# Kernel optimization log

Measured on AMD Instinct MI355X. Metric: run time of the kernel, lower is better.

Reference implementation:

```python
import jax, jax.numpy as jnp
import numpy as np

DIM = 64
N_ITER = 2
NUM_USR = 50000
NUM_ENT = 200000
NUM_REL = 32
N_NEIGHBOR = 16
BATCH = 4096


def setup_inputs() -> dict:
    key = jax.random.key(0)
    ks = jax.random.split(key, 12)
    u = jax.random.randint(ks[0], (BATCH,), 0, NUM_USR)
    v = jax.random.randint(ks[1], (BATCH,), 0, NUM_ENT)
    adj = jax.random.randint(ks[2], (NUM_ENT, N_NEIGHBOR), 0, NUM_ENT)
    rel_adj = jax.random.randint(ks[3], (NUM_ENT, N_NEIGHBOR), 0, NUM_REL + 1)
    usr_emb = jax.random.normal(ks[4], (NUM_USR, DIM), dtype=jnp.float32)
    ent_emb = jax.random.normal(ks[5], (NUM_ENT, DIM), dtype=jnp.float32)
    rel_emb = jax.random.normal(ks[6], (NUM_REL + 1, DIM), dtype=jnp.float32)
    # per-hop aggregator Linear(dim, dim) weights (applied as x @ W + b)
    scale = 1.0 / np.sqrt(DIM)
    W0 = jax.random.uniform(ks[7], (DIM, DIM), jnp.float32, -scale, scale)
    b0 = jax.random.uniform(ks[8], (DIM,), jnp.float32, -scale, scale)
    W1 = jax.random.uniform(ks[9], (DIM, DIM), jnp.float32, -scale, scale)
    b1 = jax.random.uniform(ks[10], (DIM,), jnp.float32, -scale, scale)
    return {"u": u, "v": v, "adj": adj, "rel_adj": rel_adj,
            "usr_emb": usr_emb, "ent_emb": ent_emb, "rel_emb": rel_emb,
            "W0": W0, "b0": b0, "W1": W1, "b1": b1}


def reference(u, v, adj, rel_adj, usr_emb, ent_emb, rel_emb, W0, b0, W1, b1):
    B = u.shape[0]
    user = usr_emb[u]  # [B, D]

    # multi-hop neighbor index expansion
    entities = [v[:, None]]            # hop h: [B, n^h]
    relations = []
    for h in range(N_ITER):
        ne = adj[entities[h]].reshape(B, -1)      # [B, n^(h+1)]
        nr = rel_adj[entities[h]].reshape(B, -1)
        entities.append(ne)
        relations.append(nr)

    ent_vecs = [ent_emb[e] for e in entities]     # [B, n^h, D]
    rel_vecs = [rel_emb[r] for r in relations]

    Ws, bs = [W0, W1], [b0, b1]
    for i in range(N_ITER):
        act = jnp.tanh if i == N_ITER - 1 else jax.nn.sigmoid
        nxt = []
        for hop in range(N_ITER - i):
            sv = ent_vecs[hop]                                        # [B, m, D]
            nv = ent_vecs[hop + 1].reshape(B, -1, N_NEIGHBOR, DIM)    # [B, m, n, D]
            nr = rel_vecs[hop].reshape(B, -1, N_NEIGHBOR, DIM)        # [B, m, n, D]
            # user-relation attention over neighbors
            scores = jnp.einsum('bd,bmnd->bmn', user, nr)
            attn = jax.nn.softmax(scores, axis=-1)
            agg = jnp.einsum('bmn,bmnd->bmd', attn, nv)
            out = act((sv + agg) @ Ws[i] + bs[i])
            nxt.append(out)
        ent_vecs = nxt

    item = ent_vecs[0].reshape(B, DIM)
    return jax.nn.sigmoid(jnp.sum(user * item, axis=1))
```

## Files before the change

### kernel.cpp

```cpp
#include <hip/hip_runtime.h>

#define DIMN 64
#define NNB 16
#define NREL 33
#define WPB 4
#define XSTR 68

typedef float  floatx4 __attribute__((ext_vector_type(4)));
typedef short  shortx8 __attribute__((ext_vector_type(8)));

__device__ __forceinline__ float bcastf(float x, int lane) {
    return __int_as_float(__builtin_amdgcn_readlane(__float_as_int(x), lane));
}

__global__ void prep_w0_frags(const float* __restrict__ W0, unsigned short* __restrict__ wsp) {
    const int tid = blockIdx.x * blockDim.x + threadIdx.x;
    if (tid >= 512) return;
    const int l = tid & 63;
    const int t = (tid >> 6) & 3;
    const int ks = tid >> 8;
    const int k0 = ks * 32 + (l >> 4) * 8;
    const int n  = t * 16 + (l & 15);
    const unsigned base = ((unsigned)(ks * 4 + t) * 64 + l) * 8;
    #pragma unroll
    for (int j = 0; j < 8; ++j) {
        const float x = W0[(k0 + j) * DIMN + n];
        const unsigned u  = __float_as_uint(x);
        const unsigned uh = u & 0xFFFF0000u;
        const float lf = x - __uint_as_float(uh);
        wsp[base + j]        = (unsigned short)(u >> 16);
        wsp[4096 + base + j] = (unsigned short)(__float_as_uint(lf) >> 16);
    }
}

__global__ __launch_bounds__(64 * WPB, 4)
void kgs_kernel(const int* __restrict__ u, const int* __restrict__ v,
                const int* __restrict__ adj, const int* __restrict__ rel_adj,
                const float* __restrict__ usr_emb, const float* __restrict__ ent_emb,
                const float* __restrict__ rel_emb,
                const float* __restrict__ W0, const float* __restrict__ b0,
                const float* __restrict__ W1, const float* __restrict__ b1,
                const unsigned short* __restrict__ wsp,
                float* __restrict__ out, int B)
{
    const int tid  = threadIdx.x;
    const int wid  = tid >> 6;
    const int d    = tid & 63;
    const int n16  = d & 15;
    const int quad = d >> 4;
    int b = blockIdx.x * WPB + wid;
    if (b >= B) b = B - 1;

    __shared__ __align__(16) float user_sh[WPB][DIMN];
    __shared__ float ur_sh[WPB][NREL + 3];
    __shared__ __align__(16) float sv_sh[WPB][NNB * XSTR];
    __shared__ __align__(16) float gbuf[WPB][NNB * XSTR];

    const int uu = u[b];
    const int vv = v[b];

    const float user_d = usr_emb[(size_t)uu * DIMN + d];
    const int e1n = adj[vv * NNB + n16];
    const int r1n = rel_adj[vv * NNB + n16];
    const float sv0 = ent_emb[(size_t)vv * DIMN + d];
    user_sh[wid][d] = user_d;

    floatx4 svv[4];
    #pragma unroll
    for (int q = 0; q < 4; ++q) {
        const int em = __shfl(e1n, 4 * q + quad);
        svv[q] = *(const floatx4*)(ent_emb + (size_t)em * DIMN + 4 * n16);
    }

    int e2n_r[NNB], r2n_r[NNB];
    #pragma unroll
    for (int m = 0; m < NNB; ++m) {
        const int em = __builtin_amdgcn_readlane(e1n, m);
        e2n_r[m] = adj[em * NNB + n16];
        r2n_r[m] = rel_adj[em * NNB + n16];
    }

    if (d < NREL) {
        const float* re = rel_emb + d * DIMN;
        float acc = 0.f;
        #pragma unroll
        for (int k = 0; k < DIMN; k += 4) {
            const float4 uk = *(const float4*)(&user_sh[wid][k]);
            const float4 rk = *(const float4*)(re + k);
            acc = fmaf(uk.x, rk.x, acc);
            acc = fmaf(uk.y, rk.y, acc);
            acc = fmaf(uk.z, rk.z, acc);
            acc = fmaf(uk.w, rk.w, acc);
        }
        ur_sh[wid][d] = acc;
    }

    #pragma unroll
    for (int q = 0; q < 4; ++q)
        *(floatx4*)(&sv_sh[wid][(4 * q + quad) * XSTR + 4 * n16]) = svv[q];

    float attn[NNB];
    #pragma unroll
    for (int m = 0; m < NNB; ++m) {
        const float e = __expf(ur_sh[wid][r2n_r[m]]);
        float s = e;
        s += __shfl_xor(s, 1);
        s += __shfl_xor(s, 2);
        s += __shfl_xor(s, 4);
        s += __shfl_xor(s, 8);
        attn[m] = e * __builtin_amdgcn_rcpf(s);
    }

    #pragma unroll
    for (int m = 0; m < NNB; ++m) {
        floatx4 acc4 = (floatx4){0.f, 0.f, 0.f, 0.f};
        #pragma unroll
        for (int q = 0; q < 4; ++q) {
            const int src = 4 * q + quad;
            const int en  = __shfl(e2n_r[m], src);
            const floatx4 g = *(const floatx4*)(ent_emb + (size_t)en * DIMN + 4 * n16);
            const float aw = __shfl(attn[m], src);
            acc4[0] = fmaf(aw, g[0], acc4[0]);
            acc4[1] = fmaf(aw, g[1], acc4[1]);
            acc4[2] = fmaf(aw, g[2], acc4[2]);
            acc4[3] = fmaf(aw, g[3], acc4[3]);
        }
        #pragma unroll
        for (int c = 0; c < 4; ++c) {
            acc4[c] += __shfl_xor(acc4[c], 16);
            acc4[c] += __shfl_xor(acc4[c], 32);
        }
        if (d < 16)
            *(floatx4*)(&gbuf[wid][m * XSTR + 4 * d]) = acc4;
    }

    shortx8 Ahi[2], Alo[2];
    #pragma unroll
    for (int ks = 0; ks < 2; ++ks) {
        const int off = (d & 15) * XSTR + quad * 8 + ks * 32;
        const floatx4 sa = *(const floatx4*)(&sv_sh[wid][off]);
        const floatx4 sb = *(const floatx4*)(&sv_sh[wid][off + 4]);
        const floatx4 ga = *(const floatx4*)(&gbuf[wid][off]);
        const floatx4 gb = *(const floatx4*)(&gbuf[wid][off + 4]);
        unsigned uh[8], ul[8];
        #pragma unroll
        for (int j = 0; j < 8; ++j) {
            const float x = (j < 4) ? (sa[j] + ga[j]) : (sb[j - 4] + gb[j - 4]);
            const unsigned ub = __float_as_uint(x);
            uh[j] = ub & 0xFFFF0000u;
            ul[j] = __float_as_uint(x - __uint_as_float(uh[j]));
        }
        union { int i[4]; shortx8 s; } ch, cl;
        #pragma unroll
        for (int p = 0; p < 4; ++p) {
            ch.i[p] = (int)(uh[2 * p + 1] | (uh[2 * p] >> 16));
            cl.i[p] = (int)((ul[2 * p + 1] & 0xFFFF0000u) | (ul[2 * p] >> 16));
        }
        Ahi[ks] = ch.s;
        Alo[ks] = cl.s;
    }

    const shortx8* wf = (const shortx8*)wsp;
    floatx4 acc[4];
    #pragma unroll
    for (int t = 0; t < 4; ++t) acc[t] = (floatx4){0.f, 0.f, 0.f, 0.f};
    #pragma unroll
    for (int t = 0; t < 4; ++t) {
        #pragma unroll
        for (int ks = 0; ks < 2; ++ks) {
            const int f = ks * 4 + t;
            const shortx8 bhi = wf[f * 64 + d];
            const shortx8 blo = wf[512 + f * 64 + d];
            acc[t] = __builtin_amdgcn_mfma_f32_16x16x32_bf16(Ahi[ks], bhi, acc[t], 0, 0, 0);
            acc[t] = __builtin_amdgcn_mfma_f32_16x16x32_bf16(Ahi[ks], blo, acc[t], 0, 0, 0);
            acc[t] = __builtin_amdgcn_mfma_f32_16x16x32_bf16(Alo[ks], bhi, acc[t], 0, 0, 0);
        }
    }

    #pragma unroll
    for (int t = 0; t < 4; ++t) {
        const float bv = b0[t * 16 + n16];
        #pragma unroll
        for (int reg = 0; reg < 4; ++reg) {
            const float o = acc[t][reg] + bv;
            const int m = quad * 4 + reg;
            gbuf[wid][m * XSTR + t * 16 + n16] = 1.f / (1.f + __expf(-o));
        }
    }

    const float e0 = __expf(ur_sh[wid][r1n]);
    float sum0 = e0;
    sum0 += __shfl_xor(sum0, 1);
    sum0 += __shfl_xor(sum0, 2);
    sum0 += __shfl_xor(sum0, 4);
    sum0 += __shfl_xor(sum0, 8);
    const float attn0 = e0 * __builtin_amdgcn_rcpf(sum0);

    float agg0 = 0.f, agg1 = 0.f;
    #pragma unroll
    for (int n = 0; n < NNB; ++n) {
        const float an = bcastf(attn0, n);
        agg0 = fmaf(an, sv_sh[wid][n * XSTR + d], agg0);
        agg1 = fmaf(an, gbuf[wid][n * XSTR + d], agg1);
    }

    const float x0 = sv0 + agg0;
    float a0 = 0.f, a1 = 0.f, a2 = 0.f, a3 = 0.f;
    for (int k = 0; k < DIMN; k += 4) {
        const float* wr = W0 + k * DIMN;
        a0 = fmaf(bcastf(x0, k + 0), wr[d], a0);
        a1 = fmaf(bcastf(x0, k + 1), wr[DIMN + d], a1);
        a2 = fmaf(bcastf(x0, k + 2), wr[2 * DIMN + d], a2);
        a3 = fmaf(bcastf(x0, k + 3), wr[3 * DIMN + d], a3);
    }
    const float o0 = b0[d] + ((a0 + a1) + (a2 + a3));
    const float h0 = 1.f / (1.f + __expf(-o0));

    const float x1 = h0 + agg1;
    float c0 = 0.f, c1 = 0.f, c2 = 0.f, c3 = 0.f;
    for (int k = 0; k < DIMN; k += 4) {
        const float* wr = W1 + k * DIMN;
        c0 = fmaf(bcastf(x1, k + 0), wr[d], c0);
        c1 = fmaf(bcastf(x1, k + 1), wr[DIMN + d], c1);
        c2 = fmaf(bcastf(x1, k + 2), wr[2 * DIMN + d], c2);
        c3 = fmaf(bcastf(x1, k + 3), wr[3 * DIMN + d], c3);
    }
    const float o1 = b1[d] + ((c0 + c1) + (c2 + c3));
    const float item_d = 1.f - 2.f / (1.f + __expf(2.f * o1));

    float p = user_d * item_d;
    p += __shfl_xor(p, 1);
    p += __shfl_xor(p, 2);
    p += __shfl_xor(p, 4);
    p += __shfl_xor(p, 8);
    p += __shfl_xor(p, 16);
    p += __shfl_xor(p, 32);
    if (d == 0) out[b] = 1.f / (1.f + __expf(-p));
}

extern "C" void kernel_launch(void* const* d_in, const int* in_sizes, int n_in,
                              void* d_out, int out_size, void* d_ws, size_t ws_size,
                              hipStream_t stream) {
    const int*   u       = (const int*)d_in[0];
    const int*   v       = (const int*)d_in[1];
    const int*   adj     = (const int*)d_in[2];
    const int*   rel_adj = (const int*)d_in[3];
    const float* usr_emb = (const float*)d_in[4];
    const float* ent_emb = (const float*)d_in[5];
    const float* rel_emb = (const float*)d_in[6];
    const float* W0      = (const float*)d_in[7];
    const float* b0      = (const float*)d_in[8];
    const float* W1      = (const float*)d_in[9];
    const float* b1      = (const float*)d_in[10];
    float* out = (float*)d_out;
    unsigned short* wsp = (unsigned short*)d_ws;

    const int B = in_sizes[0];
    prep_w0_frags<<<dim3(2), dim3(256), 0, stream>>>(W0, wsp);
    const int grid = (B + WPB - 1) / WPB;
    kgs_kernel<<<dim3(grid), dim3(64 * WPB), 0, stream>>>(u, v, adj, rel_adj, usr_emb,
                                                          ent_emb, rel_emb, W0, b0, W1, b1,
                                                          wsp, out, B);
}
```

Baseline: 160.7 us.

## Convert entity embeddings to fp16 each call and gather half-width rows

A prep kernel now converts the whole fp32 entity embedding table to fp16 in workspace, alongside the existing W0 fragment preparation. The main kernel is templated so its neighbor and second-hop gathers load 8-byte fp16 chunks and widen them to fp32. This targets the random-gather memory traffic, which dominates the kernel. In exchange, every call pays a full-table conversion pass (read the fp32 table, write the fp16 copy), and embedding values lose precision. The fp16 path is used only when the workspace is large enough; otherwise the kernel falls back to fp32.

Measured after the change: 156.7 us. 1.03x faster.

```diff
diff --git a/kernel.cpp b/kernel.cpp
--- a/kernel.cpp
+++ b/kernel.cpp
@@ -1,42 +1,69 @@
 #include <hip/hip_runtime.h>
+#include <hip/hip_fp16.h>
 
 #define DIMN 64
 #define NNB 16
 #define NREL 33
 #define WPB 4
 #define XSTR 68
-
-typedef float  floatx4 __attribute__((ext_vector_type(4)));
-typedef short  shortx8 __attribute__((ext_vector_type(8)));
+#define WFRAG_BYTES 16384
+
+typedef float        floatx4 __attribute__((ext_vector_type(4)));
+typedef short        shortx8 __attribute__((ext_vector_type(8)));
+typedef unsigned int uintx2  __attribute__((ext_vector_type(2)));
 
 __device__ __forceinline__ float bcastf(float x, int lane) {
     return __int_as_float(__builtin_amdgcn_readlane(__float_as_int(x), lane));
 }
 
-__global__ void prep_w0_frags(const float* __restrict__ W0, unsigned short* __restrict__ wsp) {
-    const int tid = blockIdx.x * blockDim.x + threadIdx.x;
-    if (tid >= 512) return;
-    const int l = tid & 63;
-    const int t = (tid >> 6) & 3;
-    const int ks = tid >> 8;
-    const int k0 = ks * 32 + (l >> 4) * 8;
-    const int n  = t * 16 + (l & 15);
-    const unsigned base = ((unsigned)(ks * 4 + t) * 64 + l) * 8;
-    #pragma unroll
-    for (int j = 0; j < 8; ++j) {
-        const float x = W0[(k0 + j) * DIMN + n];
-        const unsigned u  = __float_as_uint(x);
-        const unsigned uh = u & 0xFFFF0000u;
-        const float lf = x - __uint_as_float(uh);
-        wsp[base + j]        = (unsigned short)(u >> 16);
-        wsp[4096 + base + j] = (unsigned short)(__float_as_uint(lf) >> 16);
-    }
-}
-
+__global__ void prep_kernel(const float* __restrict__ W0, unsigned short* __restrict__ wsp,
+                            const float* __restrict__ ent, __half* __restrict__ ent16,
+                            long n4)
+{
+    const long tid = (long)blockIdx.x * blockDim.x + threadIdx.x;
+    if (tid < 512) {
+        const int l = (int)tid & 63;
+        const int t = ((int)tid >> 6) & 3;
+        const int ks = (int)tid >> 8;
+        const int k0 = ks * 32 + (l >> 4) * 8;
+        const int n  = t * 16 + (l & 15);
+        const unsigned base = ((unsigned)(ks * 4 + t) * 64 + l) * 8;
+        #pragma unroll
+        for (int j = 0; j < 8; ++j) {
+            const float x = W0[(k0 + j) * DIMN + n];
+            const unsigned u  = __float_as_uint(x);
+            const unsigned uh = u & 0xFFFF0000u;
+            const float lf = x - __uint_as_float(uh);
+            wsp[base + j]        = (unsigned short)(u >> 16);
+            wsp[4096 + base + j] = (unsigned short)(__float_as_uint(lf) >> 16);
+        }
+    }
+    if (ent16) {
+        const long stride = (long)gridDim.x * blockDim.x;
+        for (long i = tid; i < n4; i += stride) {
+            const float4 x = ((const float4*)ent)[i];
+            __half2 a = __floats2half2_rn(x.x, x.y);
+            __half2 b = __floats2half2_rn(x.z, x.w);
+            ((__half2*)ent16)[2 * i]     = a;
+            ((__half2*)ent16)[2 * i + 1] = b;
+        }
+    }
+}
+
+__device__ __forceinline__ floatx4 cvt4(uintx2 raw) {
+    union { unsigned int u; __half2 h; } a, b;
+    a.u = raw.x; b.u = raw.y;
+    const float2 f01 = __half22float2(a.h);
+    const float2 f23 = __half22float2(b.h);
+    return (floatx4){f01.x, f01.y, f23.x, f23.y};
+}
+
+template<bool F16>
 __global__ __launch_bounds__(64 * WPB, 4)
 void kgs_kernel(const int* __restrict__ u, const int* __restrict__ v,
                 const int* __restrict__ adj, const int* __restrict__ rel_adj,
                 const float* __restrict__ usr_emb, const float* __restrict__ ent_emb,
+                const __half* __restrict__ ent16,
                 const float* __restrict__ rel_emb,
                 const float* __restrict__ W0, const float* __restrict__ b0,
                 const float* __restrict__ W1, const float* __restrict__ b1,
@@ -62,14 +89,19 @@
     const float user_d = usr_emb[(size_t)uu * DIMN + d];
     const int e1n = adj[vv * NNB + n16];
     const int r1n = rel_adj[vv * NNB + n16];
-    const float sv0 = ent_emb[(size_t)vv * DIMN + d];
+    float sv0;
+    if constexpr (F16) sv0 = __half2float(ent16[(size_t)vv * DIMN + d]);
+    else               sv0 = ent_emb[(size_t)vv * DIMN + d];
     user_sh[wid][d] = user_d;
 
     floatx4 svv[4];
     #pragma unroll
     for (int q = 0; q < 4; ++q) {
         const int em = __shfl(e1n, 4 * q + quad);
-        svv[q] = *(const floatx4*)(ent_emb + (size_t)em * DIMN + 4 * n16);
+        if constexpr (F16)
+            svv[q] = cvt4(*(const uintx2*)(ent16 + (size_t)em * DIMN + 4 * n16));
+        else
+            svv[q] = *(const floatx4*)(ent_emb + (size_t)em * DIMN + 4 * n16);
     }
 
     int e2n_r[NNB], r2n_r[NNB];
@@ -118,7 +150,11 @@
         for (int q = 0; q < 4; ++q) {
             const int src = 4 * q + quad;
             const int en  = __shfl(e2n_r[m], src);
-            const floatx4 g = *(const floatx4*)(ent_emb + (size_t)en * DIMN + 4 * n16);
+            floatx4 g;
+            if constexpr (F16)
+                g = cvt4(*(const uintx2*)(ent16 + (size_t)en * DIMN + 4 * n16));
+            else
+                g = *(const floatx4*)(ent_emb + (size_t)en * DIMN + 4 * n16);
             const float aw = __shfl(attn[m], src);
             acc4[0] = fmaf(aw, g[0], acc4[0]);
             acc4[1] = fmaf(aw, g[1], acc4[1]);
@@ -256,9 +292,22 @@
     unsigned short* wsp = (unsigned short*)d_ws;
 
     const int B = in_sizes[0];
-    prep_w0_frags<<<dim3(2), dim3(256), 0, stream>>>(W0, wsp);
+    const long nent = (long)in_sizes[5];
+    const size_t need = (size_t)WFRAG_BYTES + (size_t)nent * sizeof(__half);
+    const bool use16 = (ws_size >= need) && ((nent & 3) == 0);
+    __half* ent16 = use16 ? (__half*)((char*)d_ws + WFRAG_BYTES) : nullptr;
+
+    const long n4 = nent / 4;
+    const int conv_blocks = use16 ? 6400 : 2;
+    prep_kernel<<<dim3(conv_blocks), dim3(256), 0, stream>>>(W0, wsp, ent_emb, ent16, n4);
+
     const int grid = (B + WPB - 1) / WPB;
-    kgs_kernel<<<dim3(grid), dim3(64 * WPB), 0, stream>>>(u, v, adj, rel_adj, usr_emb,
-                                                          ent_emb, rel_emb, W0, b0, W1, b1,
-                                                          wsp, out, B);
-}
+    if (use16)
+        kgs_kernel<true><<<dim3(grid), dim3(64 * WPB), 0, stream>>>(
+            u, v, adj, rel_adj, usr_emb, ent_emb, ent16, rel_emb, W0, b0, W1, b1,
+            wsp, out, B);
+    else
+        kgs_kernel<false><<<dim3(grid), dim3(64 * WPB), 0, stream>>>(
+            u, v, adj, rel_adj, usr_emb, ent_emb, nullptr, rel_emb, W0, b0, W1, b1,
+            wsp, out, B);
+}
```
